# Performance work log

Hardware: AMD Instinct MI355X
Metric: run time of the kernel (lower is better)

Reference implementation:

```python
import jax, jax.numpy as jnp
import numpy as np

T, F_IN, UNITS, N_CLASSES = 21, 126, 8, 27


def _run_lstm(seq, Wk, Wr, b):
    """Keras-style LSTM (gate order i,f,g,o). seq: (B,T,F) -> hs: (B,T,U)."""
    B = seq.shape[0]
    U = Wr.shape[0]
    # input projection for all timesteps at once: (B,T,4U)
    z_in = jnp.einsum('btf,fg->btg', seq, Wk) + b

    def step(carry, z_t):
        h, c = carry
        z = z_t + h @ Wr
        i, f, g, o = jnp.split(z, 4, axis=-1)
        i = jax.nn.sigmoid(i)
        f = jax.nn.sigmoid(f)
        g = jnp.tanh(g)
        o = jax.nn.sigmoid(o)
        c = f * c + i * g
        h = o * jnp.tanh(c)
        return (h, c), h

    h0 = jnp.zeros((B, U), seq.dtype)
    (_, _), hs = jax.lax.scan(step, (h0, h0), jnp.swapaxes(z_in, 0, 1))
    return jnp.swapaxes(hs, 0, 1)  # (B,T,U)


def setup_inputs() -> dict:
    key = jax.random.key(0)
    ks = jax.random.split(key, 6)
    B = 32768
    return {
        'x': jax.random.normal(ks[0], (B, T * F_IN), dtype=jnp.float32),
        'W1k': jax.random.normal(ks[1], (F_IN, 4 * UNITS), dtype=jnp.float32) * 0.1,
        'W1r': jax.random.normal(ks[2], (UNITS, 4 * UNITS), dtype=jnp.float32) * 0.1,
        'b1': jnp.zeros((4 * UNITS,), jnp.float32),
        'W2k': jax.random.normal(ks[3], (UNITS, 4 * UNITS), dtype=jnp.float32) * 0.1,
        'W2r': jax.random.normal(ks[4], (UNITS, 4 * UNITS), dtype=jnp.float32) * 0.1,
        'b2': jnp.zeros((4 * UNITS,), jnp.float32),
        'Wd': jax.random.normal(ks[5], (UNITS, N_CLASSES), dtype=jnp.float32) * 0.1,
        'bd': jnp.zeros((N_CLASSES,), jnp.float32),
    }


def reference(x, W1k, W1r, b1, W2k, W2r, b2, Wd, bd):
    B = x.shape[0]
    seq = x.reshape(B, T, F_IN)            # Reshape((21, 126))
    h1 = _run_lstm(seq, W1k, W1r, b1)      # LSTM(8, return_sequences=True)
    # dropout is identity at inference
    h2 = _run_lstm(h1, W2k, W2r, b2)[:, -1]  # LSTM(8) -> last step (B,8)
    return jax.nn.softmax(h2 @ Wd + bd)    # Dense(27, softmax)
```

## Files before the change

### kernel.cpp

```cpp
#include <hip/hip_runtime.h>


namespace {
constexpr int T_  = 21;
constexpr int FIN = 126;
constexpr int U_  = 8;
constexpr int NC  = 27;
constexpr int ZC  = 4 * U_;
constexpr int ROW = T_ * FIN;
constexpr size_t ZGRP = (size_t)T_ * ZC * 64;
}

__device__ __forceinline__ float sigm(float x) {
  return __builtin_amdgcn_rcpf(1.0f + __expf(-x));
}
__device__ __forceinline__ float tanh_f(float x) {
  return 1.0f - 2.0f * __builtin_amdgcn_rcpf(1.0f + __expf(2.0f * x));
}

__global__ __launch_bounds__(256) void zin_gemm(
    const float* __restrict__ X, const float* __restrict__ W1k,
    const float* __restrict__ b1, float* __restrict__ Z,
    int g0)
{
  __shared__ __align__(16) float xb[2][64 * FIN];

  const int tid = threadIdx.x;
  const int sl  = tid & 63;
  const int wv  = __builtin_amdgcn_readfirstlane(tid >> 6);
  const int grp = g0 + blockIdx.x;

  int  goff[16];
  int  loff[16];
  bool val[16];
  #pragma unroll
  for (int k = 0; k < 16; ++k) {
    int j = tid + k * 256;
    val[k] = (j < 64 * 63);
    int s = j / 63;
    int q = j - s * 63;
    goff[k] = s * ROW + 2 * q;
    loff[k] = s * FIN + 2 * q;
  }

  const float* xbase = X + (size_t)grp * 64 * ROW;

  const float4* Wk4 = reinterpret_cast<const float4*>(W1k) + 2 * wv;
  const float4  b1a = reinterpret_cast<const float4*>(b1)[2 * wv];
  const float4  b1b = reinterpret_cast<const float4*>(b1)[2 * wv + 1];

  float2 pf[16];
  #pragma unroll
  for (int k = 0; k < 16; ++k)
    if (val[k]) pf[k] = *reinterpret_cast<const float2*>(xbase + goff[k]);

  int p = 0;
  for (int t = 0; t < T_; ++t) {
    #pragma unroll
    for (int k = 0; k < 16; ++k)
      if (val[k]) *reinterpret_cast<float2*>(&xb[p][loff[k]]) = pf[k];
    __syncthreads();

    if (t + 1 < T_) {
      const float* xt = xbase + (t + 1) * FIN;
      #pragma unroll
      for (int k = 0; k < 16; ++k)
        if (val[k]) pf[k] = *reinterpret_cast<const float2*>(xt + goff[k]);
    }

    float4 za = b1a, zb = b1b;
    const float2* xr = reinterpret_cast<const float2*>(&xb[p][sl * FIN]);
    #pragma unroll 3
    for (int q = 0; q < 63; ++q) {
      float2 xv = xr[q];
      float4 wa0 = Wk4[(2 * q) * 8];
      float4 wb0 = Wk4[(2 * q) * 8 + 1];
      float4 wa1 = Wk4[(2 * q + 1) * 8];
      float4 wb1 = Wk4[(2 * q + 1) * 8 + 1];
      za.x = fmaf(xv.x, wa0.x, za.x); za.y = fmaf(xv.x, wa0.y, za.y);
      za.z = fmaf(xv.x, wa0.z, za.z); za.w = fmaf(xv.x, wa0.w, za.w);
      zb.x = fmaf(xv.x, wb0.x, zb.x); zb.y = fmaf(xv.x, wb0.y, zb.y);
      zb.z = fmaf(xv.x, wb0.z, zb.z); zb.w = fmaf(xv.x, wb0.w, zb.w);
      za.x = fmaf(xv.y, wa1.x, za.x); za.y = fmaf(xv.y, wa1.y, za.y);
      za.z = fmaf(xv.y, wa1.z, za.z); za.w = fmaf(xv.y, wa1.w, za.w);
      zb.x = fmaf(xv.y, wb1.x, zb.x); zb.y = fmaf(xv.y, wb1.y, zb.y);
      zb.z = fmaf(xv.y, wb1.z, zb.z); zb.w = fmaf(xv.y, wb1.w, zb.w);
    }

    float* zp = Z + (size_t)(grp - g0) * ZGRP + (size_t)t * ZC * 64
              + (size_t)(8 * wv) * 64 + sl;
    zp[0 * 64] = za.x; zp[1 * 64] = za.y; zp[2 * 64] = za.z; zp[3 * 64] = za.w;
    zp[4 * 64] = zb.x; zp[5 * 64] = zb.y; zp[6 * 64] = zb.z; zp[7 * 64] = zb.w;

    p ^= 1;
  }
}

__global__ __launch_bounds__(256) void lstm_rec(
    const float* __restrict__ Z,
    const float* __restrict__ W1r,
    const float* __restrict__ W2k, const float* __restrict__ W2r,
    const float* __restrict__ b2,
    const float* __restrict__ Wd, const float* __restrict__ bd,
    float* __restrict__ out, int g0)
{
  __shared__ __align__(16) float zb1[ZC * 64];
  __shared__ __align__(16) float zb2[ZC * 64];

  const int tid = threadIdx.x;
  const int sl  = tid & 63;
  const int wv  = __builtin_amdgcn_readfirstlane(tid >> 6);
  const int grp = g0 + blockIdx.x;

  const float* zbase = Z + (size_t)(grp - g0) * ZGRP + (size_t)(8 * wv) * 64 + sl;

  const float4 b2a = reinterpret_cast<const float4*>(b2)[2 * wv];
  const float4 b2b = reinterpret_cast<const float4*>(b2)[2 * wv + 1];

  float h1[U_], c1[U_], h2[U_], c2[U_];
  #pragma unroll
  for (int u = 0; u < U_; ++u) { h1[u] = 0.f; c1[u] = 0.f; h2[u] = 0.f; c2[u] = 0.f; }

  float zn[8], zc[8];
  #pragma unroll
  for (int c = 0; c < 8; ++c) zn[c] = zbase[c * 64];

  for (int t = 0; t < T_; ++t) {
    #pragma unroll
    for (int c = 0; c < 8; ++c) zc[c] = zn[c];
    if (t + 1 < T_) {
      const float* zt = zbase + (size_t)(t + 1) * ZC * 64;
      #pragma unroll
      for (int c = 0; c < 8; ++c) zn[c] = zt[c * 64];
    }

    float z1[8];
    #pragma unroll
    for (int c = 0; c < 8; ++c) z1[c] = zc[c];
    #pragma unroll
    for (int k = 0; k < U_; ++k) {
      float hv = h1[k];
      #pragma unroll
      for (int c = 0; c < 8; ++c)
        z1[c] = fmaf(hv, W1r[k * ZC + 8 * wv + c], z1[c]);
    }
    #pragma unroll
    for (int c = 0; c < 8; ++c) zb1[(8 * wv + c) * 64 + sl] = z1[c];
    __syncthreads();

    #pragma unroll
    for (int u = 0; u < U_; ++u) {
      float zi = zb1[u * 64 + sl];
      float zf = zb1[(U_ + u) * 64 + sl];
      float zg = zb1[(2 * U_ + u) * 64 + sl];
      float zo = zb1[(3 * U_ + u) * 64 + sl];
      float iv = sigm(zi), fv = sigm(zf), gv = tanh_f(zg), ov = sigm(zo);
      float cn = fv * c1[u] + iv * gv;
      c1[u] = cn;
      h1[u] = ov * tanh_f(cn);
    }

    float4 za = b2a, zbv = b2b;
    #pragma unroll
    for (int k = 0; k < U_; ++k) {
      float hv = h1[k];
      const float* w = &W2k[k * ZC + 8 * wv];
      za.x  = fmaf(hv, w[0], za.x);  za.y  = fmaf(hv, w[1], za.y);
      za.z  = fmaf(hv, w[2], za.z);  za.w  = fmaf(hv, w[3], za.w);
      zbv.x = fmaf(hv, w[4], zbv.x); zbv.y = fmaf(hv, w[5], zbv.y);
      zbv.z = fmaf(hv, w[6], zbv.z); zbv.w = fmaf(hv, w[7], zbv.w);
    }
    #pragma unroll
    for (int k = 0; k < U_; ++k) {
      float hv = h2[k];
      const float* w = &W2r[k * ZC + 8 * wv];
      za.x  = fmaf(hv, w[0], za.x);  za.y  = fmaf(hv, w[1], za.y);
      za.z  = fmaf(hv, w[2], za.z);  za.w  = fmaf(hv, w[3], za.w);
      zbv.x = fmaf(hv, w[4], zbv.x); zbv.y = fmaf(hv, w[5], zbv.y);
      zbv.z = fmaf(hv, w[6], zbv.z); zbv.w = fmaf(hv, w[7], zbv.w);
    }
    {
      float* zp = &zb2[(8 * wv) * 64 + sl];
      zp[0 * 64] = za.x;  zp[1 * 64] = za.y;  zp[2 * 64] = za.z;  zp[3 * 64] = za.w;
      zp[4 * 64] = zbv.x; zp[5 * 64] = zbv.y; zp[6 * 64] = zbv.z; zp[7 * 64] = zbv.w;
    }
    __syncthreads();

    #pragma unroll
    for (int u = 0; u < U_; ++u) {
      float zi = zb2[u * 64 + sl];
      float zf = zb2[(U_ + u) * 64 + sl];
      float zg = zb2[(2 * U_ + u) * 64 + sl];
      float zo = zb2[(3 * U_ + u) * 64 + sl];
      float iv = sigm(zi), fv = sigm(zf), gv = tanh_f(zg), ov = sigm(zo);
      float cn = fv * c2[u] + iv * gv;
      c2[u] = cn;
      h2[u] = ov * tanh_f(cn);
    }
  }

  float lg[NC];
  float m = -1e30f;
  #pragma unroll
  for (int c = 0; c < NC; ++c) {
    float acc = bd[c];
    #pragma unroll
    for (int k = 0; k < U_; ++k) acc = fmaf(h2[k], Wd[k * NC + c], acc);
    lg[c] = acc;
    m = fmaxf(m, acc);
  }
  float ssum = 0.f;
  #pragma unroll
  for (int c = 0; c < NC; ++c) {
    float e = __expf(lg[c] - m);
    lg[c] = e;
    ssum += e;
  }
  float inv = 1.0f / ssum;
  if (wv == 0) {
    #pragma unroll
    for (int c = 0; c < NC; ++c) zb1[sl * NC + c] = lg[c] * inv;
  }
  __syncthreads();
  {
    float* oblk = out + (size_t)grp * 64 * NC;
    #pragma unroll
    for (int k = 0; k < 7; ++k) {
      int j = tid + k * 256;
      if (j < 64 * NC) oblk[j] = zb1[j];
    }
  }
}

extern "C" void kernel_launch(void* const* d_in, const int* in_sizes, int n_in,
                              void* d_out, int out_size, void* d_ws, size_t ws_size,
                              hipStream_t stream) {
  const float* X   = (const float*)d_in[0];
  const float* W1k = (const float*)d_in[1];
  const float* W1r = (const float*)d_in[2];
  const float* b1  = (const float*)d_in[3];
  const float* W2k = (const float*)d_in[4];
  const float* W2r = (const float*)d_in[5];
  const float* b2  = (const float*)d_in[6];
  const float* Wd  = (const float*)d_in[7];
  const float* bd  = (const float*)d_in[8];
  float* out = (float*)d_out;
  float* Z   = (float*)d_ws;

  const int B    = in_sizes[0] / ROW;
  const int ngrp = B / 64;

  const size_t zgrp_bytes = ZGRP * sizeof(float);
  int gpc = (int)(ws_size / zgrp_bytes);
  if (gpc < 1) gpc = 1;
  if (gpc > ngrp) gpc = ngrp;

  for (int g0 = 0; g0 < ngrp; g0 += gpc) {
    int g1 = g0 + gpc;
    if (g1 > ngrp) g1 = ngrp;
    int n = g1 - g0;
    zin_gemm<<<dim3(n), 256, 0, stream>>>(X, W1k, b1, Z, g0);
    lstm_rec<<<dim3(n), 256, 0, stream>>>(Z, W1r, W2k, W2r, b2, Wd, bd, out, g0);
  }
}
```

Baseline: 583.2 us.

## Fuse input projection GEMM and LSTM recurrence into a single kernel

Merges the zin_gemm and lstm_rec kernels into one kernel that, per timestep, computes the input projection from shared-memory x tiles and immediately runs both LSTM layers. This drops the global-memory round trip of the Z workspace and the chunked multi-launch loop in the host code. In exchange each block now holds xb plus both gate buffers in shared memory (about 71 KB), which may reduce occupancy. The recurrent work now sits serially after the projection inside every timestep, with extra barriers.

```diff
diff --git a/kernel.cpp b/kernel.cpp
--- a/kernel.cpp
+++ b/kernel.cpp
@@ -8,7 +8,6 @@
 constexpr int NC  = 27;
 constexpr int ZC  = 4 * U_;
 constexpr int ROW = T_ * FIN;
-constexpr size_t ZGRP = (size_t)T_ * ZC * 64;
 }
 
 __device__ __forceinline__ float sigm(float x) {
@@ -18,17 +17,23 @@
   return 1.0f - 2.0f * __builtin_amdgcn_rcpf(1.0f + __expf(2.0f * x));
 }
 
-__global__ __launch_bounds__(256) void zin_gemm(
-    const float* __restrict__ X, const float* __restrict__ W1k,
-    const float* __restrict__ b1, float* __restrict__ Z,
-    int g0)
+__global__ __launch_bounds__(256) void lstm_fused(
+    const float* __restrict__ X,
+    const float* __restrict__ W1k, const float* __restrict__ b1,
+    const float* __restrict__ W1r,
+    const float* __restrict__ W2k, const float* __restrict__ W2r,
+    const float* __restrict__ b2,
+    const float* __restrict__ Wd, const float* __restrict__ bd,
+    float* __restrict__ out)
 {
   __shared__ __align__(16) float xb[2][64 * FIN];
+  __shared__ __align__(16) float zb1[ZC * 64];
+  __shared__ __align__(16) float zb2[ZC * 64];
 
   const int tid = threadIdx.x;
   const int sl  = tid & 63;
   const int wv  = __builtin_amdgcn_readfirstlane(tid >> 6);
-  const int grp = g0 + blockIdx.x;
+  const int grp = blockIdx.x;
 
   int  goff[16];
   int  loff[16];
@@ -48,6 +53,12 @@
   const float4* Wk4 = reinterpret_cast<const float4*>(W1k) + 2 * wv;
   const float4  b1a = reinterpret_cast<const float4*>(b1)[2 * wv];
   const float4  b1b = reinterpret_cast<const float4*>(b1)[2 * wv + 1];
+  const float4  b2a = reinterpret_cast<const float4*>(b2)[2 * wv];
+  const float4  b2b = reinterpret_cast<const float4*>(b2)[2 * wv + 1];
+
+  float h1[U_], c1[U_], h2[U_], c2[U_];
+  #pragma unroll
+  for (int u = 0; u < U_; ++u) { h1[u] = 0.f; c1[u] = 0.f; h2[u] = 0.f; c2[u] = 0.f; }
 
   float2 pf[16];
   #pragma unroll
@@ -68,7 +79,7 @@
         if (val[k]) pf[k] = *reinterpret_cast<const float2*>(xt + goff[k]);
     }
 
-    float4 za = b1a, zb = b1b;
+    float4 za = b1a, zbv = b1b;
     const float2* xr = reinterpret_cast<const float2*>(&xb[p][sl * FIN]);
     #pragma unroll 3
     for (int q = 0; q < 63; ++q) {
@@ -77,75 +88,31 @@
       float4 wb0 = Wk4[(2 * q) * 8 + 1];
       float4 wa1 = Wk4[(2 * q + 1) * 8];
       float4 wb1 = Wk4[(2 * q + 1) * 8 + 1];
-      za.x = fmaf(xv.x, wa0.x, za.x); za.y = fmaf(xv.x, wa0.y, za.y);
-      za.z = fmaf(xv.x, wa0.z, za.z); za.w = fmaf(xv.x, wa0.w, za.w);
-      zb.x = fmaf(xv.x, wb0.x, zb.x); zb.y = fmaf(xv.x, wb0.y, zb.y);
-      zb.z = fmaf(xv.x, wb0.z, zb.z); zb.w = fmaf(xv.x, wb0.w, zb.w);
-      za.x = fmaf(xv.y, wa1.x, za.x); za.y = fmaf(xv.y, wa1.y, za.y);
-      za.z = fmaf(xv.y, wa1.z, za.z); za.w = fmaf(xv.y, wa1.w, za.w);
-      zb.x = fmaf(xv.y, wb1.x, zb.x); zb.y = fmaf(xv.y, wb1.y, zb.y);
-      zb.z = fmaf(xv.y, wb1.z, zb.z); zb.w = fmaf(xv.y, wb1.w, zb.w);
-    }
-
-    float* zp = Z + (size_t)(grp - g0) * ZGRP + (size_t)t * ZC * 64
-              + (size_t)(8 * wv) * 64 + sl;
-    zp[0 * 64] = za.x; zp[1 * 64] = za.y; zp[2 * 64] = za.z; zp[3 * 64] = za.w;
-    zp[4 * 64] = zb.x; zp[5 * 64] = zb.y; zp[6 * 64] = zb.z; zp[7 * 64] = zb.w;
-
-    p ^= 1;
-  }
-}
-
-__global__ __launch_bounds__(256) void lstm_rec(
-    const float* __restrict__ Z,
-    const float* __restrict__ W1r,
-    const float* __restrict__ W2k, const float* __restrict__ W2r,
-    const float* __restrict__ b2,
-    const float* __restrict__ Wd, const float* __restrict__ bd,
-    float* __restrict__ out, int g0)
-{
-  __shared__ __align__(16) float zb1[ZC * 64];
-  __shared__ __align__(16) float zb2[ZC * 64];
-
-  const int tid = threadIdx.x;
-  const int sl  = tid & 63;
-  const int wv  = __builtin_amdgcn_readfirstlane(tid >> 6);
-  const int grp = g0 + blockIdx.x;
-
-  const float* zbase = Z + (size_t)(grp - g0) * ZGRP + (size_t)(8 * wv) * 64 + sl;
-
-  const float4 b2a = reinterpret_cast<const float4*>(b2)[2 * wv];
-  const float4 b2b = reinterpret_cast<const float4*>(b2)[2 * wv + 1];
-
-  float h1[U_], c1[U_], h2[U_], c2[U_];
-  #pragma unroll
-  for (int u = 0; u < U_; ++u) { h1[u] = 0.f; c1[u] = 0.f; h2[u] = 0.f; c2[u] = 0.f; }
-
-  float zn[8], zc[8];
-  #pragma unroll
-  for (int c = 0; c < 8; ++c) zn[c] = zbase[c * 64];
-
-  for (int t = 0; t < T_; ++t) {
-    #pragma unroll
-    for (int c = 0; c < 8; ++c) zc[c] = zn[c];
-    if (t + 1 < T_) {
-      const float* zt = zbase + (size_t)(t + 1) * ZC * 64;
-      #pragma unroll
-      for (int c = 0; c < 8; ++c) zn[c] = zt[c * 64];
-    }
-
-    float z1[8];
-    #pragma unroll
-    for (int c = 0; c < 8; ++c) z1[c] = zc[c];
+      za.x  = fmaf(xv.x, wa0.x, za.x);  za.y  = fmaf(xv.x, wa0.y, za.y);
+      za.z  = fmaf(xv.x, wa0.z, za.z);  za.w  = fmaf(xv.x, wa0.w, za.w);
+      zbv.x = fmaf(xv.x, wb0.x, zbv.x); zbv.y = fmaf(xv.x, wb0.y, zbv.y);
+      zbv.z = fmaf(xv.x, wb0.z, zbv.z); zbv.w = fmaf(xv.x, wb0.w, zbv.w);
+      za.x  = fmaf(xv.y, wa1.x, za.x);  za.y  = fmaf(xv.y, wa1.y, za.y);
+      za.z  = fmaf(xv.y, wa1.z, za.z);  za.w  = fmaf(xv.y, wa1.w, za.w);
+      zbv.x = fmaf(xv.y, wb1.x, zbv.x); zbv.y = fmaf(xv.y, wb1.y, zbv.y);
+      zbv.z = fmaf(xv.y, wb1.z, zbv.z); zbv.w = fmaf(xv.y, wb1.w, zbv.w);
+    }
+
     #pragma unroll
     for (int k = 0; k < U_; ++k) {
       float hv = h1[k];
-      #pragma unroll
-      for (int c = 0; c < 8; ++c)
-        z1[c] = fmaf(hv, W1r[k * ZC + 8 * wv + c], z1[c]);
-    }
-    #pragma unroll
-    for (int c = 0; c < 8; ++c) zb1[(8 * wv + c) * 64 + sl] = z1[c];
+      const float* w = &W1r[k * ZC + 8 * wv];
+      za.x  = fmaf(hv, w[0], za.x);  za.y  = fmaf(hv, w[1], za.y);
+      za.z  = fmaf(hv, w[2], za.z);  za.w  = fmaf(hv, w[3], za.w);
+      zbv.x = fmaf(hv, w[4], zbv.x); zbv.y = fmaf(hv, w[5], zbv.y);
+      zbv.z = fmaf(hv, w[6], zbv.z); zbv.w = fmaf(hv, w[7], zbv.w);
+    }
+
+    {
+      float* zp = &zb1[(8 * wv) * 64 + sl];
+      zp[0 * 64] = za.x;  zp[1 * 64] = za.y;  zp[2 * 64] = za.z;  zp[3 * 64] = za.w;
+      zp[4 * 64] = zbv.x; zp[5 * 64] = zbv.y; zp[6 * 64] = zbv.z; zp[7 * 64] = zbv.w;
+    }
     __syncthreads();
 
     #pragma unroll
@@ -160,29 +127,29 @@
       h1[u] = ov * tanh_f(cn);
     }
 
-    float4 za = b2a, zbv = b2b;
-    #pragma unroll
-    for (int k = 0; k < U_; ++k) {
-      float hv = h1[k];
-      const float* w = &W2k[k * ZC + 8 * wv];
-      za.x  = fmaf(hv, w[0], za.x);  za.y  = fmaf(hv, w[1], za.y);
-      za.z  = fmaf(hv, w[2], za.z);  za.w  = fmaf(hv, w[3], za.w);
-      zbv.x = fmaf(hv, w[4], zbv.x); zbv.y = fmaf(hv, w[5], zbv.y);
-      zbv.z = fmaf(hv, w[6], zbv.z); zbv.w = fmaf(hv, w[7], zbv.w);
-    }
-    #pragma unroll
-    for (int k = 0; k < U_; ++k) {
-      float hv = h2[k];
-      const float* w = &W2r[k * ZC + 8 * wv];
-      za.x  = fmaf(hv, w[0], za.x);  za.y  = fmaf(hv, w[1], za.y);
-      za.z  = fmaf(hv, w[2], za.z);  za.w  = fmaf(hv, w[3], za.w);
-      zbv.x = fmaf(hv, w[4], zbv.x); zbv.y = fmaf(hv, w[5], zbv.y);
-      zbv.z = fmaf(hv, w[6], zbv.z); zbv.w = fmaf(hv, w[7], zbv.w);
-    }
     {
+      float4 za2 = b2a, zb2v = b2b;
+      #pragma unroll
+      for (int k = 0; k < U_; ++k) {
+        float hv = h1[k];
+        const float* w = &W2k[k * ZC + 8 * wv];
+        za2.x  = fmaf(hv, w[0], za2.x);  za2.y  = fmaf(hv, w[1], za2.y);
+        za2.z  = fmaf(hv, w[2], za2.z);  za2.w  = fmaf(hv, w[3], za2.w);
+        zb2v.x = fmaf(hv, w[4], zb2v.x); zb2v.y = fmaf(hv, w[5], zb2v.y);
+        zb2v.z = fmaf(hv, w[6], zb2v.z); zb2v.w = fmaf(hv, w[7], zb2v.w);
+      }
+      #pragma unroll
+      for (int k = 0; k < U_; ++k) {
+        float hv = h2[k];
+        const float* w = &W2r[k * ZC + 8 * wv];
+        za2.x  = fmaf(hv, w[0], za2.x);  za2.y  = fmaf(hv, w[1], za2.y);
+        za2.z  = fmaf(hv, w[2], za2.z);  za2.w  = fmaf(hv, w[3], za2.w);
+        zb2v.x = fmaf(hv, w[4], zb2v.x); zb2v.y = fmaf(hv, w[5], zb2v.y);
+        zb2v.z = fmaf(hv, w[6], zb2v.z); zb2v.w = fmaf(hv, w[7], zb2v.w);
+      }
       float* zp = &zb2[(8 * wv) * 64 + sl];
-      zp[0 * 64] = za.x;  zp[1 * 64] = za.y;  zp[2 * 64] = za.z;  zp[3 * 64] = za.w;
-      zp[4 * 64] = zbv.x; zp[5 * 64] = zbv.y; zp[6 * 64] = zbv.z; zp[7 * 64] = zbv.w;
+      zp[0 * 64] = za2.x;  zp[1 * 64] = za2.y;  zp[2 * 64] = za2.z;  zp[3 * 64] = za2.w;
+      zp[4 * 64] = zb2v.x; zp[5 * 64] = zb2v.y; zp[6 * 64] = zb2v.z; zp[7 * 64] = zb2v.w;
     }
     __syncthreads();
 
@@ -197,6 +164,8 @@
       c2[u] = cn;
       h2[u] = ov * tanh_f(cn);
     }
+
+    p ^= 1;
   }
 
   float lg[NC];
@@ -245,21 +214,11 @@
   const float* Wd  = (const float*)d_in[7];
   const float* bd  = (const float*)d_in[8];
   float* out = (float*)d_out;
-  float* Z   = (float*)d_ws;
+  (void)d_ws; (void)ws_size;
 
   const int B    = in_sizes[0] / ROW;
   const int ngrp = B / 64;
 
-  const size_t zgrp_bytes = ZGRP * sizeof(float);
-  int gpc = (int)(ws_size / zgrp_bytes);
-  if (gpc < 1) gpc = 1;
-  if (gpc > ngrp) gpc = ngrp;
-
-  for (int g0 = 0; g0 < ngrp; g0 += gpc) {
-    int g1 = g0 + gpc;
-    if (g1 > ngrp) g1 = ngrp;
-    int n = g1 - g0;
-    zin_gemm<<<dim3(n), 256, 0, stream>>>(X, W1k, b1, Z, g0);
-    lstm_rec<<<dim3(n), 256, 0, stream>>>(Z, W1r, W2k, W2r, b2, Wd, bd, out, g0);
-  }
-}
+  lstm_fused<<<dim3(ngrp), 256, 0, stream>>>(
+      X, W1k, b1, W1r, W2k, W2r, b2, Wd, bd, out);
+}
```

Result: faster. 550.3 us (-5.6%).
